# Kernel tuning notes

Hardware: AMD Instinct MI355X
Metric: run time of the kernel (lower is better)

## Reference

```python
import jax, jax.numpy as jnp
import numpy as np
from jax import lax

EPS = 1e-6
D_MODEL = 2048
N_HEADS = 32
D_STATE = 64
HEADDIM = D_MODEL // N_HEADS  # 64, d_inner = expand*d_model = 2048
D_CONV = 4
INTER = 5504


def rmsnorm(x, w, eps=EPS):
    v = jnp.mean(jnp.square(x.astype(jnp.float32)), axis=-1, keepdims=True)
    return (x.astype(jnp.float32) * lax.rsqrt(v + eps)).astype(x.dtype) * w


def ssm_scan(x, dt, Bm, Cm):
    # x: (b,l,h,p) unscaled; dt: (b,l,h); Bm,Cm: (b,l,h,n)
    # DiscreteMamba2: h_t = exp(-dt_t) h_{t-1} + x_t (x) B_t ; y_t = h_t . C_t
    # (mamba_chunk_scan is called with x/dt and A=-1, so dt*(x/dt)=x)
    a = jnp.exp(-dt)  # (b,l,h)
    b, l, h, p = x.shape
    n = Bm.shape[-1]

    def step(hst, inp):
        a_t, x_t, B_t, C_t = inp
        hst = a_t[..., None, None] * hst + jnp.einsum('bhp,bhn->bhpn', x_t, B_t)
        y = jnp.einsum('bhpn,bhn->bhp', hst, C_t)
        return hst, y

    h0 = jnp.zeros((b, h, p, n), dtype=x.dtype)
    xs = (jnp.moveaxis(a, 1, 0), jnp.moveaxis(x, 1, 0),
          jnp.moveaxis(Bm, 1, 0), jnp.moveaxis(Cm, 1, 0))
    _, ys = lax.scan(step, h0, xs)
    return jnp.moveaxis(ys, 0, 1)  # (b,l,h,p)


def setup_inputs() -> dict:
    key = jax.random.key(0)
    ks = jax.random.split(key, 8)
    s = 0.02
    d_inner = D_MODEL
    conv_dim = d_inner + 2 * N_HEADS * D_STATE  # 6144
    d_in_proj = 2 * d_inner + 2 * N_HEADS * D_STATE + N_HEADS  # 8224
    return {
        'hidden_states': jax.random.normal(ks[0], (2, 2048, D_MODEL), jnp.float32),
        'attention_mask': jnp.ones((2, 2048), jnp.float32),
        'in_proj_w': jax.random.normal(ks[1], (d_in_proj, D_MODEL), jnp.float32) * s,
        'conv_w': jax.random.normal(ks[2], (conv_dim, 1, D_CONV), jnp.float32) * s,
        'conv_b': jnp.zeros((conv_dim,), jnp.float32),
        'z_bias': jnp.zeros((d_inner,), jnp.float32),
        'D': jnp.ones((N_HEADS,), jnp.float32),
        'out_proj_w': jax.random.normal(ks[3], (D_MODEL, d_inner), jnp.float32) * s,
        'ln1_w': jnp.ones((D_MODEL,), jnp.float32),
        'ln2_w': jnp.ones((D_MODEL,), jnp.float32),
        'gate_w': jax.random.normal(ks[4], (INTER, D_MODEL), jnp.float32) * s,
        'up_w': jax.random.normal(ks[5], (INTER, D_MODEL), jnp.float32) * s,
        'down_w': jax.random.normal(ks[6], (D_MODEL, INTER), jnp.float32) * s,
    }


def reference(hidden_states, attention_mask, in_proj_w, conv_w, conv_b, z_bias,
              D, out_proj_w, ln1_w, ln2_w, gate_w, up_w, down_w):
    b, l, d_model = hidden_states.shape
    d_inner = z_bias.shape[0]
    h_heads = D.shape[0]
    conv_dim = conv_w.shape[0]
    d_state = (conv_dim - d_inner) // (2 * h_heads)
    headdim = d_inner // h_heads

    residual = hidden_states
    h = rmsnorm(hidden_states, ln1_w)
    h = h * attention_mask[..., None]

    # --- DiscreteMamba2 mixer ---
    zxbcdt = jnp.einsum('bld,ed->ble', h, in_proj_w)
    z = zxbcdt[..., :d_inner]
    xBC = zxbcdt[..., d_inner:d_inner + conv_dim]
    A_log = zxbcdt[..., d_inner + conv_dim:]  # (b,l,h)

    # causal depthwise conv (activation = identity)
    xc = jnp.pad(jnp.swapaxes(xBC, 1, 2), ((0, 0), (0, 0), (conv_w.shape[-1] - 1, 0)))
    xBC = lax.conv_general_dilated(xc, conv_w, (1,), 'VALID',
                                   dimension_numbers=('NCH', 'OIH', 'NCH'),
                                   feature_group_count=conv_dim)
    xBC = jnp.swapaxes(xBC + conv_b[None, :, None], 1, 2)  # (b,l,conv_dim)

    x = xBC[..., :d_inner].reshape(b, l, h_heads, headdim)
    Bm = xBC[..., d_inner:d_inner + h_heads * d_state].reshape(b, l, h_heads, d_state)
    Cm = xBC[..., d_inner + h_heads * d_state:].reshape(b, l, h_heads, d_state)

    dt = jax.nn.softplus(A_log)  # (b,l,h)
    y = ssm_scan(x, dt, Bm, Cm)
    y = y + D[None, None, :, None] * x  # D skip uses unscaled x
    y = y.reshape(b, l, d_inner)

    gated = y * jax.nn.silu(z + z_bias)
    mixer_out = jnp.einsum('bld,ed->ble', gated, out_proj_w)

    h = mixer_out + residual
    residual2 = h
    h = rmsnorm(h, ln2_w)
    mlp = jnp.einsum('bli,di->bld',
                     jax.nn.silu(jnp.einsum('bld,id->bli', h, gate_w)) *
                     jnp.einsum('bld,id->bli', h, up_w),
                     down_w)
    return residual2 + mlp
```

## Files before the change

kernel.cpp:

```cpp
#include <hip/hip_runtime.h>
#include <math.h>

typedef __bf16 bf16_t;
typedef __attribute__((ext_vector_type(8))) __bf16 bf16x8;
typedef __attribute__((ext_vector_type(4))) float f32x4;

#define D_MODEL   2048
#define L_SEQ     2048
#define BATCH     2
#define NTOK      4096
#define N_HEADS   32
#define D_STATE   64
#define HEADDIM   64
#define D_INNER   2048
#define CONV_DIM  6144
#define D_IN_PROJ 8224
#define INTER     5504
#define QCHUNK    128
#define KCHUNKS   16

__device__ __forceinline__ void gld_lds16(const void* g, void* l) {
    __builtin_amdgcn_global_load_lds(
        (const __attribute__((address_space(1))) unsigned int*)g,
        (__attribute__((address_space(3))) unsigned int*)l, 16, 0, 0);
}

__global__ __launch_bounds__(256) void cvt_kernel(
    const float* __restrict__ s, bf16_t* __restrict__ d, int n8)
{
    int i = blockIdx.x * 256 + threadIdx.x;
    if (i >= n8) return;
    const float4* s4 = (const float4*)s;
    float4 a = s4[2 * i], b = s4[2 * i + 1];
    bf16x8 r;
    r[0] = (bf16_t)a.x; r[1] = (bf16_t)a.y; r[2] = (bf16_t)a.z; r[3] = (bf16_t)a.w;
    r[4] = (bf16_t)b.x; r[5] = (bf16_t)b.y; r[6] = (bf16_t)b.z; r[7] = (bf16_t)b.w;
    ((bf16x8*)d)[i] = r;
}

__global__ __launch_bounds__(256) void rmsnorm_kernel(
    const float* __restrict__ x, const float* __restrict__ w,
    const float* __restrict__ mask, bf16_t* __restrict__ out)
{
    __shared__ float red[4];
    __shared__ float sinv;
    int row = blockIdx.x;
    const float* xr = x + (size_t)row * D_MODEL;
    float xv[8];
    float ss = 0.f;
#pragma unroll
    for (int i = 0; i < 8; ++i) {
        float v = xr[threadIdx.x + 256 * i];
        xv[i] = v;
        ss += v * v;
    }
    for (int off = 32; off >= 1; off >>= 1) ss += __shfl_down(ss, off, 64);
    int lane = threadIdx.x & 63, wv = threadIdx.x >> 6;
    if (lane == 0) red[wv] = ss;
    __syncthreads();
    if (threadIdx.x == 0) {
        float t = red[0] + red[1] + red[2] + red[3];
        sinv = rsqrtf(t / (float)D_MODEL + 1e-6f);
    }
    __syncthreads();
    float s = sinv;
    float m = mask ? mask[row] : 1.f;
    bf16_t* orow = out + (size_t)row * D_MODEL;
#pragma unroll
    for (int i = 0; i < 8; ++i) {
        int c = threadIdx.x + 256 * i;
        orow[c] = (bf16_t)(xv[i] * s * w[c] * m);
    }
}

template <bool RES, typename OT>
__global__ __launch_bounds__(256) void gemm_bt(
    const bf16_t* __restrict__ X, const bf16_t* __restrict__ W,
    const float* __restrict__ R, OT* __restrict__ O,
    int N, int K, int ldo)
{
    __shared__ __attribute__((aligned(16))) bf16_t As[128 * 32];
    __shared__ __attribute__((aligned(16))) bf16_t Bs[128 * 32];

    int tid = threadIdx.x;
    int m0 = blockIdx.y * 128;
    int n0 = blockIdx.x * 128;

    f32x4 acc[4][4] = {};

    int lane = tid & 63;
    int wv = tid >> 6;
    int wm = (wv >> 1) * 64, wn = (wv & 1) * 64;
    int lm = lane & 15, lq = lane >> 4;

    int srow = tid >> 2;
    int scol = (tid & 3) * 8;
    const bf16_t* Xp0 = X + (size_t)(m0 + srow) * K + scol;
    const bf16_t* Xp1 = X + (size_t)(m0 + 64 + srow) * K + scol;
    int wr0 = n0 + srow;      if (wr0 > N - 1) wr0 = N - 1;
    int wr1 = n0 + 64 + srow; if (wr1 > N - 1) wr1 = N - 1;
    const bf16_t* Wp0 = W + (size_t)wr0 * K + scol;
    const bf16_t* Wp1 = W + (size_t)wr1 * K + scol;
    bf16_t* lA0 = &As[tid * 8];
    bf16_t* lA1 = &As[2048 + tid * 8];
    bf16_t* lB0 = &Bs[tid * 8];
    bf16_t* lB1 = &Bs[2048 + tid * 8];

    for (int k0 = 0; k0 < K; k0 += 32) {
        __syncthreads();
        gld_lds16(Xp0 + k0, lA0);
        gld_lds16(Xp1 + k0, lA1);
        gld_lds16(Wp0 + k0, lB0);
        gld_lds16(Wp1 + k0, lB1);
        __syncthreads();

        bf16x8 a[4], b[4];
#pragma unroll
        for (int i = 0; i < 4; ++i)
            a[i] = *(const bf16x8*)&As[(wm + i * 16 + lm) * 32 + lq * 8];
#pragma unroll
        for (int i = 0; i < 4; ++i)
            b[i] = *(const bf16x8*)&Bs[(wn + i * 16 + lm) * 32 + lq * 8];
#pragma unroll
        for (int mi = 0; mi < 4; ++mi)
#pragma unroll
            for (int ni = 0; ni < 4; ++ni)
                acc[mi][ni] = __builtin_amdgcn_mfma_f32_16x16x32_bf16(
                    a[mi], b[ni], acc[mi][ni], 0, 0, 0);
    }

#pragma unroll
    for (int mi = 0; mi < 4; ++mi)
#pragma unroll
        for (int ni = 0; ni < 4; ++ni) {
            int n = n0 + wn + ni * 16 + lm;
            if (n >= N) continue;
            int mbase = m0 + wm + mi * 16 + lq * 4;
#pragma unroll
            for (int r = 0; r < 4; ++r) {
                size_t off = (size_t)(mbase + r) * ldo + n;
                float v = acc[mi][ni][r];
                if (RES) v += R[off];
                O[off] = (OT)v;
            }
        }
}


#define G8_BARRIER() do { asm volatile("" ::: "memory"); \
    __builtin_amdgcn_s_barrier(); \
    asm volatile("" ::: "memory"); } while (0)
#define G8_LGKM0() do { asm volatile("s_waitcnt lgkmcnt(0)" ::: "memory"); \
    __builtin_amdgcn_sched_barrier(0); } while (0)
#define G8_VMCNT(n) asm volatile("s_waitcnt vmcnt(" #n ")" ::: "memory")

template <int C>
__device__ __forceinline__ void g8_stage(
    int t, int nt4, const bf16_t* pA, size_t hK64,
    const bf16_t* pB0, const bf16_t* pB1, const bf16_t* pB2, const bf16_t* pB3,
    unsigned dbase, bf16_t* lds)
{
    constexpr int w = C & 3;
    constexpr unsigned so = (((C >> 2) & 1) ? 65536u : 0u) + (unsigned)w * 16384u;
    int j = 8 * t + C;
    if (j >= nt4) return;
    size_t goff = (size_t)(j >> 2) * 64;
    const bf16_t *g0, *g1;
    if constexpr (w == 0)      { g0 = pA;              g1 = pA + hK64; }
    else if constexpr (w == 1) { g0 = pA + 2 * hK64;   g1 = pA + 3 * hK64; }
    else if constexpr (w == 2) { g0 = pB0;             g1 = pB1; }
    else                       { g0 = pB2;             g1 = pB3; }
    gld_lds16(g0 + goff, (char*)lds + (so + dbase));
    gld_lds16(g1 + goff, (char*)lds + (so + 8192u + dbase));
}

template <bool RES, typename OT>
__global__ __launch_bounds__(512, 2) void gemm8p(
    const bf16_t* __restrict__ X, const bf16_t* __restrict__ W,
    const float* __restrict__ R, OT* __restrict__ O,
    int N, int K, int ldo)
{
    __shared__ __attribute__((aligned(1024))) bf16_t lds[65536];

    const int tid  = threadIdx.x;
    const int lane = tid & 63;
    const int wid  = tid >> 6;
    const int wr   = wid >> 2;
    const int wc   = wid & 3;

    int nx   = gridDim.x;
    int nwg  = nx * gridDim.y;
    int orig = blockIdx.x + nx * blockIdx.y;
    int qx = nwg >> 3, rx = nwg & 7;
    int xcd = orig & 7, l8 = orig >> 3;
    int wg = (xcd < rx ? xcd * (qx + 1) : rx * (qx + 1) + (xcd - rx) * qx) + l8;
    int m0 = (wg / nx) * 256;
    int n0 = (wg % nx) * 256;

    const int NT    = K >> 6;
    const int nt4   = NT << 2;
    const int niter = NT >> 1;

    int lrow = ((tid >> 7) << 4) + ((tid >> 2) & 15);
    int cb   = (tid & 3) * 16;
    int cblg = cb ^ (((tid >> 2) & 8) ? 32 : 0);
    int lcol = (((tid >> 6) & 1) << 5) + (cblg >> 1);
    const size_t hK64 = (size_t)K << 6;
    const bf16_t* pA = X + (size_t)(m0 + lrow) * K + lcol;
    const bf16_t* pB[4];
#pragma unroll
    for (int hi = 0; hi < 4; ++hi) {
        int rw = n0 + (hi >> 1) * 128 + (hi & 1) * 64 + lrow;
        if (rw > N - 1) rw = N - 1;
        pB[hi] = W + (size_t)rw * K + lcol;
    }
    const unsigned dbase = (unsigned)tid * 16u;

    unsigned c2s = ((unsigned)(lane >> 4) << 4) ^ ((lane & 8) ? 32u : 0u);
    unsigned rdA = (unsigned)(wr * 16384 + (lane & 15) * 64) + c2s;
    unsigned rdB = 32768u + (unsigned)((wc >> 1) * 16384 + (wc & 1) * 8192
                                       + (lane & 15) * 64) + c2s;

    f32x4 acc[8][4] = {};
    bf16x8 a[8][2], b[4][2];

#define G8_STG(C) g8_stage<C>(t, nt4, pA, hK64, pB[0], pB[1], pB[2], pB[3], dbase, lds)
#define G8_LDFRAGS(SO) do { \
    const char* pa_ = (const char*)lds + (SO) + rdA; \
    const char* pb_ = (const char*)lds + (SO) + rdB; \
    _Pragma("unroll") for (int mi = 0; mi < 8; ++mi) { \
        a[mi][0] = *(const bf16x8*)(pa_ + mi * 2048); \
        a[mi][1] = *(const bf16x8*)(pa_ + mi * 2048 + 1024); } \
    _Pragma("unroll") for (int ni = 0; ni < 4; ++ni) { \
        b[ni][0] = *(const bf16x8*)(pb_ + ni * 2048); \
        b[ni][1] = *(const bf16x8*)(pb_ + ni * 2048 + 1024); } \
} while (0)
#define G8_MFMAQ(MI0, NI0) do { \
    __builtin_amdgcn_s_setprio(1); \
    _Pragma("unroll") for (int mi = 0; mi < 4; ++mi) \
    _Pragma("unroll") for (int ni = 0; ni < 2; ++ni) \
    _Pragma("unroll") for (int ks = 0; ks < 2; ++ks) \
        acc[(MI0) + mi][(NI0) + ni] = __builtin_amdgcn_mfma_f32_16x16x32_bf16( \
            a[(MI0) + mi][ks], b[(NI0) + ni][ks], acc[(MI0) + mi][(NI0) + ni], 0, 0, 0); \
    __builtin_amdgcn_s_setprio(0); \
} while (0)

    {
        int t = 0;
        G8_STG(0); G8_STG(1); G8_STG(2); G8_STG(3);
        G8_STG(4); G8_STG(5); G8_STG(6);
    }
    G8_VMCNT(6);
    G8_BARRIER();

#pragma unroll 1
    for (int t = 0; t < niter; ++t) {
        G8_STG(7);
        G8_LDFRAGS(0u);
        G8_BARRIER(); G8_LGKM0();
        G8_MFMAQ(0, 0);
        G8_BARRIER();
        G8_STG(8);
        G8_BARRIER();
        G8_MFMAQ(0, 2);
        G8_BARRIER();
        G8_STG(9);
        G8_BARRIER();
        G8_MFMAQ(4, 0);
        G8_BARRIER();
        G8_STG(10);
        if (t == niter - 1) { G8_VMCNT(0); } else { G8_VMCNT(6); }
        G8_BARRIER();
        G8_MFMAQ(4, 2);
        G8_BARRIER();
        G8_STG(11);
        G8_LDFRAGS(65536u);
        G8_BARRIER(); G8_LGKM0();
        G8_MFMAQ(0, 0);
        G8_BARRIER();
        G8_STG(12);
        G8_BARRIER();
        G8_MFMAQ(0, 2);
        G8_BARRIER();
        G8_STG(13);
        G8_BARRIER();
        G8_MFMAQ(4, 0);
        G8_BARRIER();
        G8_STG(14);
        G8_VMCNT(6);
        G8_BARRIER();
        G8_MFMAQ(4, 2);
        G8_BARRIER();
    }

#undef G8_STG
#undef G8_LDFRAGS
#undef G8_MFMAQ

#pragma unroll
    for (int mi = 0; mi < 8; ++mi)
#pragma unroll
        for (int ni = 0; ni < 4; ++ni) {
            int n = n0 + wc * 64 + ni * 16 + (lane & 15);
            if (n >= N) continue;
            int mbase = m0 + wr * 128 + mi * 16 + (lane >> 4) * 4;
#pragma unroll
            for (int r = 0; r < 4; ++r) {
                size_t off = (size_t)(mbase + r) * ldo + n;
                float v = acc[mi][ni][r];
                if (RES) v += R[off];
                O[off] = (OT)v;
            }
        }
}

__global__ __launch_bounds__(256) void conv_kernel(
    const bf16_t* __restrict__ zx, const float* __restrict__ cw,
    const float* __restrict__ cb, bf16_t* __restrict__ out)
{
    int c = blockIdx.x * 256 + threadIdx.x;
    int l0 = blockIdx.y * 128;
    int b = blockIdx.z;
    float w0 = cw[c * 4 + 0], w1 = cw[c * 4 + 1];
    float w2 = cw[c * 4 + 2], w3 = cw[c * 4 + 3];
    float bias = cb[c];
    const bf16_t* src = zx + (size_t)b * L_SEQ * D_IN_PROJ + 2048 + c;
    bf16_t* dst = out + (size_t)b * L_SEQ * CONV_DIM + c;
    float xm3 = (l0 >= 3) ? (float)src[(size_t)(l0 - 3) * D_IN_PROJ] : 0.f;
    float xm2 = (l0 >= 2) ? (float)src[(size_t)(l0 - 2) * D_IN_PROJ] : 0.f;
    float xm1 = (l0 >= 1) ? (float)src[(size_t)(l0 - 1) * D_IN_PROJ] : 0.f;
    for (int l = l0; l < l0 + 128; ++l) {
        float xc = (float)src[(size_t)l * D_IN_PROJ];
        float r = bias + xm3 * w0 + xm2 * w1 + xm1 * w2 + xc * w3;
        dst[(size_t)l * CONV_DIM] = (bf16_t)r;
        xm3 = xm2; xm2 = xm1; xm1 = xc;
    }
}

__global__ __launch_bounds__(256) void scan_state_kernel(
    const bf16_t* __restrict__ conv, const bf16_t* __restrict__ zx,
    float* __restrict__ Schunk, float* __restrict__ Aprod)
{
    const int SS = 32;
    __shared__ __attribute__((aligned(16))) float xs[SS][64];
    __shared__ __attribute__((aligned(16))) float bs[SS][64];
    __shared__ float as_[SS];

    int k = blockIdx.x, h = blockIdx.y, b = blockIdx.z;
    int tid = threadIdx.x, lane = tid & 63, wv = tid >> 6;
    int pt = tid >> 3, nt = tid & 7;
    int p0 = pt * 2, n0 = nt * 8;

    float st0[8] = {0, 0, 0, 0, 0, 0, 0, 0};
    float st1[8] = {0, 0, 0, 0, 0, 0, 0, 0};
    float aprod = 1.f;

    const bf16_t* cbase = conv + (size_t)b * L_SEQ * CONV_DIM + h * 64;
    const bf16_t* abase = zx + (size_t)b * L_SEQ * D_IN_PROJ + 8192 + h;

    int tstart = k * QCHUNK;
    for (int t0 = tstart; t0 < tstart + QCHUNK; t0 += SS) {
        int soff = (wv >> 1) * 16;
        for (int s = 0; s < 16; ++s) {
            size_t row = (size_t)(t0 + soff + s);
            if ((wv & 1) == 0) xs[soff + s][lane] = (float)cbase[row * CONV_DIM + lane];
            else               bs[soff + s][lane] = (float)cbase[row * CONV_DIM + 2048 + lane];
        }
        if (tid < SS) {
            float v = (float)abase[(size_t)(t0 + tid) * D_IN_PROJ];
            as_[tid] = 1.f / (1.f + __expf(v));
        }
        __syncthreads();
        for (int s = 0; s < SS; ++s) {
            float a = as_[s];
            float x0 = xs[s][p0], x1 = xs[s][p0 + 1];
            aprod *= a;
#pragma unroll
            for (int j = 0; j < 8; ++j) {
                float Bv = bs[s][n0 + j];
                st0[j] = a * st0[j] + x0 * Bv;
                st1[j] = a * st1[j] + x1 * Bv;
            }
        }
        __syncthreads();
    }
    size_t base = (((size_t)(b * N_HEADS + h)) * KCHUNKS + k) * 4096;
    float4* d0 = (float4*)&Schunk[base + p0 * 64 + n0];
    d0[0] = make_float4(st0[0], st0[1], st0[2], st0[3]);
    d0[1] = make_float4(st0[4], st0[5], st0[6], st0[7]);
    float4* d1 = (float4*)&Schunk[base + (p0 + 1) * 64 + n0];
    d1[0] = make_float4(st1[0], st1[1], st1[2], st1[3]);
    d1[1] = make_float4(st1[4], st1[5], st1[6], st1[7]);
    if (tid == 0) Aprod[(b * N_HEADS + h) * KCHUNKS + k] = aprod;
}

__global__ __launch_bounds__(256) void scan_combine_kernel(
    const float* __restrict__ Schunk, const float* __restrict__ Aprod,
    float* __restrict__ Sinit)
{
    int bh = blockIdx.x >> 4;
    int e = (blockIdx.x & 15) * 256 + threadIdx.x;
    size_t base = (size_t)bh * KCHUNKS * 4096 + e;
    float S = 0.f;
    for (int k = 0; k < KCHUNKS; ++k) {
        Sinit[base + (size_t)k * 4096] = S;
        float ap = Aprod[bh * KCHUNKS + k];
        S = ap * S + Schunk[base + (size_t)k * 4096];
    }
}

__global__ __launch_bounds__(256) void scan_out_kernel(
    const bf16_t* __restrict__ conv, const bf16_t* __restrict__ zx,
    const float* __restrict__ Sinit, const float* __restrict__ Dp,
    const float* __restrict__ zb, bf16_t* __restrict__ gated)
{
    const int S = 16;
    __shared__ __attribute__((aligned(16))) float xs[S][64];
    __shared__ __attribute__((aligned(16))) float bs[S][64];
    __shared__ __attribute__((aligned(16))) float cs[S][64];
    __shared__ __attribute__((aligned(16))) float zs[S][64];
    __shared__ float as_[S];

    int k = blockIdx.x, h = blockIdx.y, b = blockIdx.z;
    int tid = threadIdx.x;
    int lane = tid & 63, wv = tid >> 6;
    int pt = tid >> 3, nt = tid & 7;
    int p0 = pt * 2, n0 = nt * 8;

    size_t sbase = (((size_t)(b * N_HEADS + h)) * KCHUNKS + k) * 4096;
    float4 v00 = *(const float4*)&Sinit[sbase + p0 * 64 + n0];
    float4 v01 = *(const float4*)&Sinit[sbase + p0 * 64 + n0 + 4];
    float4 v10 = *(const float4*)&Sinit[sbase + (p0 + 1) * 64 + n0];
    float4 v11 = *(const float4*)&Sinit[sbase + (p0 + 1) * 64 + n0 + 4];
    float st0[8] = {v00.x, v00.y, v00.z, v00.w, v01.x, v01.y, v01.z, v01.w};
    float st1[8] = {v10.x, v10.y, v10.z, v10.w, v11.x, v11.y, v11.z, v11.w};

    float Dh  = Dp[h];
    float zb0 = zb[h * 64 + p0];
    float zb1 = zb[h * 64 + p0 + 1];

    const bf16_t* cbase = conv + (size_t)b * L_SEQ * CONV_DIM + h * 64;
    const bf16_t* zbase = zx + (size_t)b * L_SEQ * D_IN_PROJ + h * 64;
    const bf16_t* abase = zx + (size_t)b * L_SEQ * D_IN_PROJ + 8192 + h;
    bf16_t* obase = gated + (size_t)b * L_SEQ * D_INNER + h * 64;

    int tstart = k * QCHUNK;
    for (int t0 = tstart; t0 < tstart + QCHUNK; t0 += S) {
        for (int s = 0; s < S; ++s) {
            size_t row = (size_t)(t0 + s);
            if (wv == 0)      xs[s][lane] = (float)cbase[row * CONV_DIM + lane];
            else if (wv == 1) bs[s][lane] = (float)cbase[row * CONV_DIM + 2048 + lane];
            else if (wv == 2) cs[s][lane] = (float)cbase[row * CONV_DIM + 4096 + lane];
            else              zs[s][lane] = (float)zbase[row * D_IN_PROJ + lane];
        }
        if (tid < S) {
            float v = (float)abase[(size_t)(t0 + tid) * D_IN_PROJ];
            as_[tid] = 1.f / (1.f + __expf(v));
        }
        __syncthreads();

        for (int s = 0; s < S; ++s) {
            float a = as_[s];
            float x0 = xs[s][p0], x1 = xs[s][p0 + 1];
            float part0 = 0.f, part1 = 0.f;
#pragma unroll
            for (int j = 0; j < 8; ++j) {
                float Bv = bs[s][n0 + j];
                float Cv = cs[s][n0 + j];
                st0[j] = a * st0[j] + x0 * Bv;
                st1[j] = a * st1[j] + x1 * Bv;
                part0 += st0[j] * Cv;
                part1 += st1[j] * Cv;
            }
            for (int o = 1; o < 8; o <<= 1) {
                part0 += __shfl_xor(part0, o, 64);
                part1 += __shfl_xor(part1, o, 64);
            }
            if (nt == 0) {
                float y0 = part0 + Dh * x0;
                float y1 = part1 + Dh * x1;
                float z0 = zs[s][p0] + zb0;
                float z1 = zs[s][p0 + 1] + zb1;
                y0 *= z0 / (1.f + __expf(-z0));
                y1 *= z1 / (1.f + __expf(-z1));
                bf16_t* o2 = obase + (size_t)(t0 + s) * D_INNER + p0;
                o2[0] = (bf16_t)y0;
                o2[1] = (bf16_t)y1;
            }
        }
        __syncthreads();
    }
}

__global__ __launch_bounds__(256) void act_kernel(
    const bf16_t* __restrict__ gu, bf16_t* __restrict__ act, int n8)
{
    int i = blockIdx.x * 256 + threadIdx.x;
    if (i >= n8) return;
    int row = i / (INTER / 8);
    int c8  = i % (INTER / 8);
    const bf16x8* g = (const bf16x8*)(gu + (size_t)row * (2 * INTER)) + c8;
    const bf16x8* u = (const bf16x8*)(gu + (size_t)row * (2 * INTER) + INTER) + c8;
    bf16x8 gv = *g, uv = *u, r;
#pragma unroll
    for (int j = 0; j < 8; ++j) {
        float x = (float)gv[j];
        r[j] = (bf16_t)((x / (1.f + __expf(-x))) * (float)uv[j]);
    }
    ((bf16x8*)act)[i] = r;
}

extern "C" void kernel_launch(void* const* d_in, const int* in_sizes, int n_in,
                              void* d_out, int out_size, void* d_ws, size_t ws_size,
                              hipStream_t stream) {
    const float* hidden     = (const float*)d_in[0];
    const float* mask       = (const float*)d_in[1];
    const float* in_proj_w  = (const float*)d_in[2];
    const float* conv_w     = (const float*)d_in[3];
    const float* conv_b     = (const float*)d_in[4];
    const float* z_bias     = (const float*)d_in[5];
    const float* Dvec       = (const float*)d_in[6];
    const float* out_proj_w = (const float*)d_in[7];
    const float* ln1_w      = (const float*)d_in[8];
    const float* ln2_w      = (const float*)d_in[9];
    const float* gate_w     = (const float*)d_in[10];
    const float* up_w       = (const float*)d_in[11];
    const float* down_w     = (const float*)d_in[12];
    float* out = (float*)d_out;

    char* ws = (char*)d_ws;
    bf16_t* zxb    = (bf16_t*)(ws + 0);
    bf16_t* convo  = (bf16_t*)(ws + 67371008);
    bf16_t* hn     = (bf16_t*)(ws + 117702656);
    bf16_t* gated  = (bf16_t*)(ws + 117702656);
    float*  Schunk = (float*) (ws + 134479872);
    bf16_t* wbuf   = (bf16_t*)(ws + 151257088);
    float*  Sinit  = (float*) (ws + 151257088);
    float*  Aprod  = (float*) (ws + 168034304);
    bf16_t* guO    = (bf16_t*)(ws + 0);
    bf16_t* guW    = (bf16_t*)(ws + 90177536);
    bf16_t* actO   = (bf16_t*)(ws + 90177536);
    bf16_t* h2n    = (bf16_t*)(ws + 135266304);
    bf16_t* dwW    = (bf16_t*)(ws + 135266304);

    rmsnorm_kernel<<<NTOK, 256, 0, stream>>>(hidden, ln1_w, mask, hn);
    cvt_kernel<<<8224, 256, 0, stream>>>(in_proj_w, wbuf, D_IN_PROJ * D_MODEL / 8);
    gemm8p<false, bf16_t><<<dim3(32, 16), 512, 0, stream>>>(
        hn, wbuf, nullptr, zxb, 8192, D_MODEL, D_IN_PROJ);
    gemm_bt<false, bf16_t><<<dim3(1, 32), 256, 0, stream>>>(
        hn, wbuf + (size_t)8192 * D_MODEL, nullptr, zxb + 8192, 32, D_MODEL, D_IN_PROJ);
    conv_kernel<<<dim3(24, 16, 2), 256, 0, stream>>>(zxb, conv_w, conv_b, convo);
    scan_state_kernel<<<dim3(KCHUNKS, N_HEADS, BATCH), 256, 0, stream>>>(convo, zxb, Schunk, Aprod);
    scan_combine_kernel<<<1024, 256, 0, stream>>>(Schunk, Aprod, Sinit);
    scan_out_kernel<<<dim3(KCHUNKS, N_HEADS, BATCH), 256, 0, stream>>>(convo, zxb, Sinit, Dvec, z_bias, gated);
    cvt_kernel<<<2048, 256, 0, stream>>>(out_proj_w, wbuf, D_MODEL * D_INNER / 8);
    gemm_bt<true, float><<<dim3(16, 32), 256, 0, stream>>>(
        gated, wbuf, hidden, out, D_MODEL, D_INNER, D_MODEL);
    rmsnorm_kernel<<<NTOK, 256, 0, stream>>>(out, ln2_w, nullptr, h2n);
    cvt_kernel<<<5504, 256, 0, stream>>>(gate_w, guW, INTER * D_MODEL / 8);
    cvt_kernel<<<5504, 256, 0, stream>>>(up_w, guW + (size_t)INTER * D_MODEL, INTER * D_MODEL / 8);
    gemm8p<false, bf16_t><<<dim3(43, 16), 512, 0, stream>>>(
        h2n, guW, nullptr, guO, 2 * INTER, D_MODEL, 2 * INTER);
    act_kernel<<<11008, 256, 0, stream>>>(guO, actO, NTOK * INTER / 8);
    cvt_kernel<<<5504, 256, 0, stream>>>(down_w, dwW, D_MODEL * INTER / 8);
    gemm_bt<true, float><<<dim3(16, 32), 256, 0, stream>>>(
        actO, dwW, out, out, D_MODEL, INTER, D_MODEL);
}
```

Before: 1.176 ms.

## Split LDS fragment loads per quadrant and reorder GEMM staging to free registers

The 256x256 GEMM main loop now loads A and B fragments from LDS incrementally, once per MFMA quadrant, instead of loading every fragment up front. This halves the A fragment register array. The global-to-LDS staging order changes to load B before A, with a shallower prefetch depth (vmcnt 4 instead of 6). The aim is lower register pressure and LDS reads interleaved with MFMA work. In exchange there are more LDS wait points per iteration and less global prefetch in flight, so memory latency may be hidden less well.

```diff
diff --git a/kernel.cpp b/kernel.cpp
--- a/kernel.cpp
+++ b/kernel.cpp
@@ -154,21 +154,19 @@
     __builtin_amdgcn_sched_barrier(0); } while (0)
 #define G8_VMCNT(n) asm volatile("s_waitcnt vmcnt(" #n ")" ::: "memory")
 
-template <int C>
+template <int W>
 __device__ __forceinline__ void g8_stage(
-    int t, int nt4, const bf16_t* pA, size_t hK64,
+    int tile, int NT, const bf16_t* pA, size_t hK64,
     const bf16_t* pB0, const bf16_t* pB1, const bf16_t* pB2, const bf16_t* pB3,
     unsigned dbase, bf16_t* lds)
 {
-    constexpr int w = C & 3;
-    constexpr unsigned so = (((C >> 2) & 1) ? 65536u : 0u) + (unsigned)w * 16384u;
-    int j = 8 * t + C;
-    if (j >= nt4) return;
-    size_t goff = (size_t)(j >> 2) * 64;
+    if (tile >= NT) return;
+    unsigned so = ((tile & 1) ? 65536u : 0u) + (unsigned)W * 16384u;
+    size_t goff = (size_t)tile * 64;
     const bf16_t *g0, *g1;
-    if constexpr (w == 0)      { g0 = pA;              g1 = pA + hK64; }
-    else if constexpr (w == 1) { g0 = pA + 2 * hK64;   g1 = pA + 3 * hK64; }
-    else if constexpr (w == 2) { g0 = pB0;             g1 = pB1; }
+    if constexpr (W == 0)      { g0 = pA;              g1 = pA + hK64; }
+    else if constexpr (W == 1) { g0 = pA + 2 * hK64;   g1 = pA + 3 * hK64; }
+    else if constexpr (W == 2) { g0 = pB0;             g1 = pB1; }
     else                       { g0 = pB2;             g1 = pB3; }
     gld_lds16(g0 + goff, (char*)lds + (so + dbase));
     gld_lds16(g1 + goff, (char*)lds + (so + 8192u + dbase));
@@ -198,7 +196,6 @@
     int n0 = (wg % nx) * 256;
 
     const int NT    = K >> 6;
-    const int nt4   = NT << 2;
     const int niter = NT >> 1;
 
     int lrow = ((tid >> 7) << 4) + ((tid >> 2) & 15);
@@ -222,18 +219,21 @@
                                        + (lane & 15) * 64) + c2s;
 
     f32x4 acc[8][4] = {};
-    bf16x8 a[8][2], b[4][2];
-
-#define G8_STG(C) g8_stage<C>(t, nt4, pA, hK64, pB[0], pB[1], pB[2], pB[3], dbase, lds)
-#define G8_LDFRAGS(SO) do { \
-    const char* pa_ = (const char*)lds + (SO) + rdA; \
-    const char* pb_ = (const char*)lds + (SO) + rdB; \
-    _Pragma("unroll") for (int mi = 0; mi < 8; ++mi) { \
+    bf16x8 a[4][2], b[4][2];
+
+#define G8_STG(W_, TILE) g8_stage<W_>((TILE), NT, pA, hK64, \
+    pB[0], pB[1], pB[2], pB[3], dbase, lds)
+#define G8_LDA(SO, HI) do { \
+    const char* pa_ = (const char*)lds + (SO) + rdA + (HI) * 8192; \
+    _Pragma("unroll") for (int mi = 0; mi < 4; ++mi) { \
         a[mi][0] = *(const bf16x8*)(pa_ + mi * 2048); \
         a[mi][1] = *(const bf16x8*)(pa_ + mi * 2048 + 1024); } \
-    _Pragma("unroll") for (int ni = 0; ni < 4; ++ni) { \
-        b[ni][0] = *(const bf16x8*)(pb_ + ni * 2048); \
-        b[ni][1] = *(const bf16x8*)(pb_ + ni * 2048 + 1024); } \
+} while (0)
+#define G8_LDB(SO, NI0) do { \
+    const char* pb_ = (const char*)lds + (SO) + rdB + (NI0) * 2048; \
+    _Pragma("unroll") for (int nj = 0; nj < 2; ++nj) { \
+        b[(NI0) + nj][0] = *(const bf16x8*)(pb_ + nj * 2048); \
+        b[(NI0) + nj][1] = *(const bf16x8*)(pb_ + nj * 2048 + 1024); } \
 } while (0)
 #define G8_MFMAQ(MI0, NI0) do { \
     __builtin_amdgcn_s_setprio(1); \
@@ -241,60 +241,63 @@
     _Pragma("unroll") for (int ni = 0; ni < 2; ++ni) \
     _Pragma("unroll") for (int ks = 0; ks < 2; ++ks) \
         acc[(MI0) + mi][(NI0) + ni] = __builtin_amdgcn_mfma_f32_16x16x32_bf16( \
-            a[(MI0) + mi][ks], b[(NI0) + ni][ks], acc[(MI0) + mi][(NI0) + ni], 0, 0, 0); \
+            a[mi][ks], b[(NI0) + ni][ks], acc[(MI0) + mi][(NI0) + ni], 0, 0, 0); \
     __builtin_amdgcn_s_setprio(0); \
 } while (0)
 
-    {
-        int t = 0;
-        G8_STG(0); G8_STG(1); G8_STG(2); G8_STG(3);
-        G8_STG(4); G8_STG(5); G8_STG(6);
-    }
-    G8_VMCNT(6);
+    G8_STG(2, 0); G8_STG(3, 0); G8_STG(0, 0); G8_STG(1, 0);
+    G8_STG(2, 1); G8_STG(3, 1);
+    G8_VMCNT(4);
     G8_BARRIER();
 
 #pragma unroll 1
     for (int t = 0; t < niter; ++t) {
-        G8_STG(7);
-        G8_LDFRAGS(0u);
+        const int t2 = 2 * t;
+        G8_STG(0, t2 + 1);
+        G8_LDA(0u, 0); G8_LDB(0u, 0);
         G8_BARRIER(); G8_LGKM0();
         G8_MFMAQ(0, 0);
         G8_BARRIER();
-        G8_STG(8);
-        G8_BARRIER();
+        G8_STG(1, t2 + 1);
+        G8_LDB(0u, 2);
+        G8_BARRIER(); G8_LGKM0();
         G8_MFMAQ(0, 2);
         G8_BARRIER();
-        G8_STG(9);
-        G8_BARRIER();
+        G8_STG(2, t2 + 2);
+        G8_LDA(0u, 1);
+        G8_BARRIER(); G8_LGKM0();
         G8_MFMAQ(4, 0);
         G8_BARRIER();
-        G8_STG(10);
-        if (t == niter - 1) { G8_VMCNT(0); } else { G8_VMCNT(6); }
+        G8_STG(3, t2 + 2);
+        if (t == niter - 1) { G8_VMCNT(0); } else { G8_VMCNT(4); }
         G8_BARRIER();
         G8_MFMAQ(4, 2);
         G8_BARRIER();
-        G8_STG(11);
-        G8_LDFRAGS(65536u);
+        G8_STG(0, t2 + 2);
+        G8_LDA(65536u, 0); G8_LDB(65536u, 0);
         G8_BARRIER(); G8_LGKM0();
         G8_MFMAQ(0, 0);
         G8_BARRIER();
-        G8_STG(12);
-        G8_BARRIER();
+        G8_STG(1, t2 + 2);
+        G8_LDB(65536u, 2);
+        G8_BARRIER(); G8_LGKM0();
         G8_MFMAQ(0, 2);
         G8_BARRIER();
-        G8_STG(13);
-        G8_BARRIER();
+        G8_STG(2, t2 + 3);
+        G8_LDA(65536u, 1);
+        G8_BARRIER(); G8_LGKM0();
         G8_MFMAQ(4, 0);
         G8_BARRIER();
-        G8_STG(14);
-        G8_VMCNT(6);
+        G8_STG(3, t2 + 3);
+        G8_VMCNT(4);
         G8_BARRIER();
         G8_MFMAQ(4, 2);
         G8_BARRIER();
     }
 
 #undef G8_STG
-#undef G8_LDFRAGS
+#undef G8_LDA
+#undef G8_LDB
 #undef G8_MFMAQ
 
 #pragma unroll
```

New measurement: 1.041 ms. 1.13x faster.
